# Kernel optimization log

Measured on AMD Instinct MI355X. Metric: run time of the kernel, lower is better.

## Reference

```python
import jax, jax.numpy as jnp
import numpy as np

B, T, D = 2, 2048, 2048
N, K, H = 16, 8, 128            # heads, kv heads, head_dim
SOFT_CAP = 50.0
WINDOW = 1024
SCALE = H ** -0.5               # query_pre_attn_scalar
ROPE_BASE = 10000.0
ROPE_SCALE = 1.0
K_MASK = -2.3819763e+38


def rms_norm(x, scale, eps=1e-6):
    var = jnp.mean(jnp.square(x), axis=-1, keepdims=True)
    return x * jax.lax.rsqrt(var + eps) * (1.0 + scale)


def apply_rope(x, positions):
    # x: [B,T,heads,H]; positions: [B,T] int
    head_dim = x.shape[-1]
    fraction = 2.0 * jnp.arange(head_dim // 2, dtype=jnp.float32) / head_dim
    timescale = ROPE_BASE ** fraction                      # [H/2]
    sinusoid = positions[..., None].astype(jnp.float32) / timescale  # [B,T,H/2]
    sinusoid = sinusoid[..., None, :] / ROPE_SCALE          # [B,T,1,H/2]
    sin, cos = jnp.sin(sinusoid), jnp.cos(sinusoid)
    first, second = jnp.split(x, 2, axis=-1)
    return jnp.concatenate([first * cos - second * sin,
                            second * cos + first * sin], axis=-1)


def setup_inputs() -> dict:
    key = jax.random.key(0)
    ks = jax.random.split(key, 6)
    x = jax.random.normal(ks[0], (B, T, D), jnp.float32)
    q_w = jax.random.normal(ks[1], (N, D, H), jnp.float32) * (D ** -0.5)
    kv_w = jax.random.normal(ks[2], (2, K, D, H), jnp.float32) * (D ** -0.5)
    o_w = jax.random.normal(ks[3], (N, H, D), jnp.float32) * ((N * H) ** -0.5)
    qnorm_scale = 0.1 * jax.random.normal(ks[4], (H,), jnp.float32)
    knorm_scale = 0.1 * jax.random.normal(ks[5], (H,), jnp.float32)
    segment_pos = jnp.broadcast_to(jnp.arange(T, dtype=jnp.int32), (B, T))
    attn_mask = jnp.broadcast_to(jnp.tril(jnp.ones((T, T), dtype=bool)), (B, T, T))
    return {"x": x, "q_w": q_w, "kv_w": kv_w, "o_w": o_w,
            "qnorm_scale": qnorm_scale, "knorm_scale": knorm_scale,
            "segment_pos": segment_pos, "attn_mask": attn_mask}


def reference(x, q_w, kv_w, o_w, qnorm_scale, knorm_scale, segment_pos, attn_mask):
    # projections
    q = jnp.einsum('BTD,NDH->BTNH', x, q_w)            # [B,T,N,H]
    k = jnp.einsum('BSD,KDH->BSKH', x, kv_w[0])        # [B,T,K,H]
    v = jnp.einsum('BSD,KDH->BSKH', x, kv_w[1])
    # QK RMSNorm, then RoPE, then query scaling (matches source order)
    q = apply_rope(rms_norm(q, qnorm_scale), segment_pos) * SCALE
    k = apply_rope(rms_norm(k, knorm_scale), segment_pos)
    # GQA: regroup query heads per kv head
    G = N // K
    qg = q.reshape(B, T, K, G, H)
    logits = jnp.einsum('BTKGH,BSKH->BTKGS', qg, k).reshape(B, T, N, T)
    # logit soft cap
    logits = jnp.tanh(logits / SOFT_CAP) * SOFT_CAP
    # sliding window mask combined with causal attn_mask
    pos_q = segment_pos[:, :, None]
    pos_k = segment_pos[:, None, :]
    sliding = (pos_k > pos_q - WINDOW) & (pos_k < pos_q + WINDOW)
    mask = attn_mask & sliding                          # [B,T,S]
    padded = jnp.where(mask[:, :, None, :], logits, K_MASK)
    probs = jax.nn.softmax(padded, axis=-1).astype(k.dtype)
    enc = jnp.einsum('BTKGS,BSKH->BTKGH',
                     probs.reshape(B, T, K, G, T), v).reshape(B, T, N, H)
    return jnp.einsum('BTNH,NHD->BTD', enc, o_w)
```

## Files before the change

### kernel.cpp

```cpp
#include <hip/hip_runtime.h>
#include <stdint.h>

#define BB 2
#define TT 2048
#define DD 2048
#define NHD 16
#define KVH 8
#define HD 128
#define JC 4096
#define WIN 1024
#define SCALE_Q 0.08838834764831845f

typedef __attribute__((ext_vector_type(8))) short bf16x8;
typedef __attribute__((ext_vector_type(8))) unsigned short us8;
typedef __attribute__((ext_vector_type(4))) unsigned short us4;
typedef __attribute__((ext_vector_type(4))) float f32x4;
typedef __attribute__((ext_vector_type(16))) float f32x16;
typedef __attribute__((ext_vector_type(4))) unsigned int u32x4;

#define GAS __attribute__((address_space(1)))
#define LAS __attribute__((address_space(3)))

__device__ __forceinline__ unsigned short f2bf(float f) {
  unsigned u = __float_as_uint(f);
  u += 0x7FFFu + ((u >> 16) & 1u);
  return (unsigned short)(u >> 16);
}
__device__ __forceinline__ float bf2f(unsigned short u) {
  return __uint_as_float(((unsigned)u) << 16);
}

__device__ __forceinline__ void gload16(const void* g, void* l) {
  __builtin_amdgcn_global_load_lds((const GAS unsigned int*)g, (LAS unsigned int*)l, 16, 0, 0);
}

#define VMCNT(n) asm volatile("s_waitcnt vmcnt(" #n ")" ::: "memory")

__global__ void __launch_bounds__(256) k_pre(
    const float4* __restrict__ x4, us4* __restrict__ xb,
    const float* __restrict__ qw, const float* __restrict__ kvw,
    const float* __restrict__ ow, unsigned short* __restrict__ Wt,
    unsigned short* __restrict__ Wt_o) {
  __shared__ float tile[32][33];
  int id = blockIdx.x;
  int tid = threadIdx.x;
  if (id < 8192) {
    int i = id * 256 + tid;
    float4 v = x4[i];
    us4 o;
    o[0] = f2bf(v.x); o[1] = f2bf(v.y); o[2] = f2bf(v.z); o[3] = f2bf(v.w);
    xb[i] = o;
    return;
  }
  const float* ib;
  unsigned short* ob;
  int ldin, c0, r0;
  int t = id - 8192;
  if (t < 8192) {
    int bx = t & 3, by = (t >> 2) & 63, z = t >> 8;
    ib = (z < 16) ? qw + (long)z * 2048 * 128 : kvw + (long)(z - 16) * 2048 * 128;
    ob = Wt + (long)z * 128 * 2048;
    ldin = 128;
    c0 = bx * 32; r0 = by * 32;
  } else {
    int u = t - 8192;
    ib = ow; ob = Wt_o; ldin = 2048;
    c0 = (u & 63) * 32; r0 = (u >> 6) * 32;
  }
  int tx = tid & 31, ty = tid >> 5;
#pragma unroll
  for (int i = 0; i < 4; i++)
    tile[ty + i * 8][tx] = ib[(long)(r0 + ty + i * 8) * ldin + c0 + tx];
  __syncthreads();
#pragma unroll
  for (int i = 0; i < 4; i++)
    ob[(long)(c0 + ty + i * 8) * 2048 + r0 + tx] = f2bf(tile[tx][ty + i * 8]);
}

template <int BM, int BN, int NWN, int THREADS, int NBUF, bool BF16OUT>
__global__ void __launch_bounds__(THREADS, 2) k_gemm9(
    const unsigned short* __restrict__ A, const unsigned short* __restrict__ Bt,
    void* __restrict__ Cv, int M, int Nn, int nby) {
  constexpr int KD = 2048;
  constexpr int NT = KD / 32;
  constexpr int ROWS = BM + BN;
  constexpr int RPI = THREADS / 4;
  constexpr int IA = BM / RPI;
  constexpr int IPT = ROWS / RPI;
  constexpr int MT = BM / 32;
  constexpr int MT2 = MT / 2;
  __shared__ short lds[NBUF][ROWS * 32];

  int tid = threadIdx.x, lane = tid & 63, w = tid >> 6;
  int wm = w / NWN, wn = w % NWN;
  int id = blockIdx.x;
  int cpx = gridDim.x >> 3;
  id = (id & 7) * cpx + (id >> 3);
  int m0 = (id / nby) * BM, n0 = (id % nby) * BN;

  int srow = tid >> 2;
  int scol = ((tid & 3) ^ ((tid >> 3) & 3)) * 8;
  const unsigned short* gA = A + (long)(m0 + srow) * KD + scol;
  const unsigned short* gB = Bt + (long)(n0 + srow) * KD + scol;

  auto STG = [&](int p, int ko, int j) {
    if (j < IA)
      gload16(gA + (long)j * RPI * KD + ko, &lds[p][(j * RPI + w * 16) * 32]);
    else
      gload16(gB + (long)(j - IA) * RPI * KD + ko,
              &lds[p][(BM + (j - IA) * RPI + w * 16) * 32]);
  };

  int frag = (lane & 15) * 32 + (((lane >> 4) ^ ((lane >> 1) & 3)) * 8);
  int abase = wm * (BM / 2) * 32 + frag;
  int bbase = (BM + wn * 64) * 32 + frag;

  f32x4 acc[MT][4] = {};
#pragma unroll
  for (int tt = 0; tt < NBUF - 1; ++tt)
#pragma unroll
    for (int j = 0; j < IPT; ++j) STG(tt, tt * 32, j);
  {
    constexpr int PW = IPT * (NBUF - 2);
    if constexpr (PW >= 8)      VMCNT(8);
    else if constexpr (PW == 6) VMCNT(6);
    else if constexpr (PW == 4) VMCNT(4);
    else                        VMCNT(0);
  }
  __builtin_amdgcn_s_barrier();

  int buf = 0, sp = NBUF - 1;
  for (int t = 0; t < NT; ++t) {
    const short* bufp = lds[buf];
    bool st = (t + NBUF - 1) < NT;
    int ko = (t + NBUF - 1) * 32;
    bf16x8 bfr[4], af[MT2];
#pragma unroll
    for (int ni = 0; ni < 4; ++ni)
      bfr[ni] = *(const bf16x8*)&bufp[bbase + ni * 16 * 32];
#pragma unroll
    for (int mi = 0; mi < MT2; ++mi)
      af[mi] = *(const bf16x8*)&bufp[abase + mi * 16 * 32];
    if (st) {
#pragma unroll
      for (int j = 0; j < IPT / 2; ++j) STG(sp, ko, j);
    }
    __builtin_amdgcn_s_barrier();
    asm volatile("s_waitcnt lgkmcnt(0)" ::: "memory");
    __builtin_amdgcn_sched_barrier(0);
    __builtin_amdgcn_s_setprio(1);
#pragma unroll
    for (int mi = 0; mi < MT2; ++mi)
#pragma unroll
      for (int ni = 0; ni < 4; ++ni)
        acc[mi][ni] = __builtin_amdgcn_mfma_f32_16x16x32_bf16(af[mi], bfr[ni], acc[mi][ni], 0, 0, 0);
    __builtin_amdgcn_s_setprio(0);
    __builtin_amdgcn_s_barrier();
    bf16x8 af2[MT2];
#pragma unroll
    for (int mi = 0; mi < MT2; ++mi)
      af2[mi] = *(const bf16x8*)&bufp[abase + (MT2 + mi) * 16 * 32];
    if (st) {
#pragma unroll
      for (int j = IPT / 2; j < IPT; ++j) STG(sp, ko, j);
    }
    {
      int rem = NT - 2 - t;
      if (rem > NBUF - 2) rem = NBUF - 2;
      if (rem == 2) {
        if constexpr (IPT == 4) VMCNT(8); else VMCNT(12);
      } else if (rem == 1) {
        if constexpr (IPT == 4) VMCNT(4); else VMCNT(6);
      } else if (rem == 0) {
        VMCNT(0);
      }
    }
    __builtin_amdgcn_s_barrier();
    asm volatile("s_waitcnt lgkmcnt(0)" ::: "memory");
    __builtin_amdgcn_sched_barrier(0);
    __builtin_amdgcn_s_setprio(1);
#pragma unroll
    for (int mi = 0; mi < MT2; ++mi)
#pragma unroll
      for (int ni = 0; ni < 4; ++ni)
        acc[MT2 + mi][ni] = __builtin_amdgcn_mfma_f32_16x16x32_bf16(af2[mi], bfr[ni], acc[MT2 + mi][ni], 0, 0, 0);
    __builtin_amdgcn_s_setprio(0);
    __builtin_amdgcn_s_barrier();
    buf = (buf == NBUF - 1) ? 0 : buf + 1;
    sp = (sp == NBUF - 1) ? 0 : sp + 1;
  }

#pragma unroll
  for (int mi = 0; mi < MT; mi++)
#pragma unroll
    for (int ni = 0; ni < 4; ni++)
#pragma unroll
      for (int r = 0; r < 4; r++) {
        int row = m0 + wm * (BM / 2) + mi * 16 + (lane >> 4) * 4 + r;
        int col = n0 + wn * 64 + ni * 16 + (lane & 15);
        if constexpr (BF16OUT)
          ((unsigned short*)Cv)[(long)row * Nn + col] = f2bf(acc[mi][ni][r]);
        else
          ((float*)Cv)[(long)row * Nn + col] = acc[mi][ni][r];
      }
}

__global__ void __launch_bounds__(256) k_post(
    const unsigned short* __restrict__ qkv, const float* __restrict__ qns,
    const float* __restrict__ kns, unsigned short* __restrict__ qb,
    unsigned short* __restrict__ kb, unsigned short* __restrict__ vbT) {
  int id = blockIdx.x;
  int tid = threadIdx.x;
  if (id < 24576) {
    int wid = tid >> 6, lane = tid & 63;
    long r = (long)id * 4 + wid;
    int b = (int)(r / (TT * 24));
    int rem = (int)(r % (TT * 24));
    int t = rem / 24, hd = rem % 24;
    const unsigned short* row = qkv + (long)(b * TT + t) * JC + (hd < 16 ? hd * HD : 2048 + (hd - 16) * HD);
    float f0 = bf2f(row[lane]), f1 = bf2f(row[lane + 64]);
    float ss = f0 * f0 + f1 * f1;
#pragma unroll
    for (int m = 1; m < 64; m <<= 1) ss += __shfl_xor(ss, m, 64);
    float rinv = rsqrtf(ss * (1.0f / 128.0f) + 1e-6f);
    const float* sc = (hd < 16) ? qns : kns;
    float y0 = f0 * rinv * (1.0f + sc[lane]);
    float y1 = f1 * rinv * (1.0f + sc[lane + 64]);
    float ts = exp2f((float)lane * (13.287712379549449f / 64.0f));
    float ang = (float)t / ts;
    float s, c;
    sincosf(ang, &s, &c);
    float o0 = y0 * c - y1 * s;
    float o1 = y1 * c + y0 * s;
    unsigned short* dst;
    if (hd < 16) {
      o0 *= SCALE_Q; o1 *= SCALE_Q;
      dst = qb + ((long)(b * NHD + hd) * TT + t) * HD;
    } else {
      dst = kb + ((long)(b * KVH + (hd - 16)) * TT + t) * HD;
    }
    dst[lane] = f2bf(o0);
    dst[lane + 64] = f2bf(o1);
    return;
  }
  __shared__ unsigned short tile[32][33];
  int t4 = id - 24576;
  int bx = t4 & 3, by = (t4 >> 2) & 63, z = t4 >> 8;
  const unsigned short* ib = qkv + 3072 + (long)(z / 8) * 2048 * 4096 + (long)(z % 8) * 128;
  unsigned short* ob = vbT + (long)z * 128 * 2048;
  int c0 = bx * 32, r0 = by * 32;
  int tx = tid & 31, ty = tid >> 5;
#pragma unroll
  for (int i = 0; i < 4; i++)
    tile[ty + i * 8][tx] = ib[(long)(r0 + ty + i * 8) * 4096 + c0 + tx];
  __syncthreads();
#pragma unroll
  for (int i = 0; i < 4; i++)
    ob[(long)(c0 + ty + i * 8) * 2048 + r0 + tx] = tile[tx][ty + i * 8];
}

template <bool FULL>
__device__ __forceinline__ void softcap16(const f32x16& s16, float* pr, float& lsum,
                                          int s_base, int tq, int g) {
#pragma unroll
  for (int r = 0; r < 16; r++) {
    float x = s16[r];
    float e2 = __builtin_amdgcn_exp2f(0.05770780163555853f * x);
    float p = __builtin_amdgcn_exp2f(-144.26950408889634f * __builtin_amdgcn_rcpf(1.0f + e2));
    if (!FULL) {
      int s = s_base + (r & 3) + 8 * (r >> 2) + 4 * g;
      bool valid = (s <= tq) && (s > tq - WIN);
      p = valid ? p : 0.0f;
    }
    lsum += p;
    pr[r] = p;
  }
}

__device__ __forceinline__ void hswap(unsigned& a, unsigned& b, int g) {
  unsigned ax = (unsigned)__shfl_xor((int)a, 32, 64);
  unsigned bx = (unsigned)__shfl_xor((int)b, 32, 64);
  unsigned r0 = g ? bx : a;
  unsigned r1 = g ? b : ax;
  a = r0; b = r1;
}

__global__ void __launch_bounds__(256, 2) k_attn(
    const unsigned short* __restrict__ qb, const unsigned short* __restrict__ kb,
    const unsigned short* __restrict__ vbT, unsigned short* __restrict__ enc) {
  __shared__ short Kl[2][64][128];
  __shared__ short Vt[2][128][64];
  int tid = threadIdx.x, lane = tid & 63, w = tid >> 6;
  int g = lane >> 5, l31 = lane & 31;
  int id = blockIdx.x;
  int b = id >> 8;
  int rem = id & 255;
  int n = rem >> 4;
  int traw = rem & 15;
  int tile = b ? ((traw + 8) & 15) : traw;
  int t0 = tile * 128;
  int kh = n >> 1;
  const unsigned short* qbase = qb + ((long)(b * NHD + n) * TT + t0 + w * 32) * HD;
  const unsigned short* kbase = kb + (long)(b * KVH + kh) * TT * HD;
  const unsigned short* vbase = vbT + (long)(b * KVH + kh) * HD * TT;

  bf16x8 bq[8];
  {
    const unsigned short* qp = qbase + (long)l31 * HD + g * 8;
#pragma unroll
    for (int kb8 = 0; kb8 < 8; kb8++)
      bq[kb8] = *(const bf16x8*)(qp + kb8 * 16);
  }

  f32x16 acc[4] = {};
  float lsum = 0.0f;
  int t0w = t0 + w * 32;
  int tq = t0w + l31;
  int s_begin = (t0 >= WIN) ? t0 - WIN : 0;
  int s_end = t0 + 128;

  auto STAGE = [&](int buf, int s0) {
#pragma unroll
    for (int i = 0; i < 4; i++) {
      int row = w * 16 + i * 4 + (lane >> 4);
      int c16 = (lane & 15) ^ (row & 7);
      gload16(kbase + (long)(s0 + row) * HD + c16 * 8, &Kl[buf][w * 16 + i * 4][0]);
    }
#pragma unroll
    for (int i = 0; i < 4; i++) {
      int row = w * 32 + i * 8 + (lane >> 3);
      int c16 = (lane & 7) ^ (row & 7);
      gload16(vbase + (long)row * TT + s0 + c16 * 8, &Vt[buf][w * 32 + i * 8][0]);
    }
  };

  STAGE(0, s_begin);
  __syncthreads();
  int cur = 0;
  for (int s0 = s_begin; s0 < s_end; s0 += 64) {
    if (s0 + 64 < s_end) STAGE(cur ^ 1, s0 + 64);
    bool live = (s0 <= t0w + 31) && (s0 + 63 >= t0w - (WIN - 1));
    if (live) {
      f32x16 sc2[2] = {};
#pragma unroll
      for (int sb = 0; sb < 2; sb++) {
        int srow = sb * 32 + l31;
#pragma unroll
        for (int kb8 = 0; kb8 < 8; kb8++) {
          bf16x8 ak = *(const bf16x8*)&Kl[cur][srow][8 * ((2 * kb8 + g) ^ (srow & 7))];
          sc2[sb] = __builtin_amdgcn_mfma_f32_32x32x16_bf16(ak, bq[kb8], sc2[sb], 0, 0, 0);
        }
      }
      bool full = (s0 + 63 <= t0w) && (s0 >= t0w + 31 - (WIN - 1));
      unsigned pw[4][4];
#pragma unroll
      for (int sb = 0; sb < 2; sb++) {
        float pr[16];
        if (full) softcap16<true>(sc2[sb], pr, lsum, 0, tq, g);
        else      softcap16<false>(sc2[sb], pr, lsum, s0 + sb * 32, tq, g);
        unsigned X[4], Y[4];
#pragma unroll
        for (int m = 0; m < 4; m++) {
          asm("v_cvt_pk_bf16_f32 %0, %1, %2" : "=v"(X[m]) : "v"(pr[4 * m]), "v"(pr[4 * m + 1]));
          asm("v_cvt_pk_bf16_f32 %0, %1, %2" : "=v"(Y[m]) : "v"(pr[4 * m + 2]), "v"(pr[4 * m + 3]));
        }
#pragma unroll
        for (int kl = 0; kl < 2; kl++) {
          hswap(X[2 * kl], X[2 * kl + 1], g);
          hswap(Y[2 * kl], Y[2 * kl + 1], g);
          pw[sb * 2 + kl][0] = X[2 * kl];
          pw[sb * 2 + kl][1] = Y[2 * kl];
          pw[sb * 2 + kl][2] = X[2 * kl + 1];
          pw[sb * 2 + kl][3] = Y[2 * kl + 1];
        }
      }
#pragma unroll
      for (int ks = 0; ks < 4; ks++) {
        u32x4 t4 = {pw[ks][0], pw[ks][1], pw[ks][2], pw[ks][3]};
        bf16x8 pb = __builtin_bit_cast(bf16x8, t4);
#pragma unroll
        for (int ht = 0; ht < 4; ht++) {
          int hrow = ht * 32 + l31;
          bf16x8 av = *(const bf16x8*)&Vt[cur][hrow][8 * ((2 * ks + g) ^ (hrow & 7))];
          acc[ht] = __builtin_amdgcn_mfma_f32_32x32x16_bf16(av, pb, acc[ht], 0, 0, 0);
        }
      }
    }
    __syncthreads();
    cur ^= 1;
  }

  lsum += __shfl_xor(lsum, 32, 64);
  float inv = __builtin_amdgcn_rcpf(lsum);
  unsigned short* dst = enc + ((long)(b * TT + tq) * NHD + n) * HD;
#pragma unroll
  for (int ht = 0; ht < 4; ht++)
#pragma unroll
    for (int r4 = 0; r4 < 4; r4++) {
      us4 o;
#pragma unroll
      for (int e = 0; e < 4; e++) o[e] = f2bf(acc[ht][r4 * 4 + e] * inv);
      *(us4*)(dst + ht * 32 + 8 * r4 + 4 * g) = o;
    }
}

extern "C" void kernel_launch(void* const* d_in, const int* in_sizes, int n_in,
                              void* d_out, int out_size, void* d_ws, size_t ws_size,
                              hipStream_t stream) {
  const float* x    = (const float*)d_in[0];
  const float* q_w  = (const float*)d_in[1];
  const float* kv_w = (const float*)d_in[2];
  const float* o_w  = (const float*)d_in[3];
  const float* qns  = (const float*)d_in[4];
  const float* kns  = (const float*)d_in[5];

  if (ws_size < (104ull << 20)) return;
  char* ws = (char*)d_ws;
  unsigned short* qkvb = (unsigned short*)(ws + 0);
  unsigned short* enc  = (unsigned short*)(ws + 0);
  unsigned short* x_bf = (unsigned short*)(ws + (64ll << 20));
  unsigned short* qb   = (unsigned short*)(ws + (64ll << 20));
  unsigned short* Wt   = (unsigned short*)(ws + (80ll << 20));
  unsigned short* kb   = (unsigned short*)(ws + (80ll << 20));
  unsigned short* vbT  = (unsigned short*)(ws + (88ll << 20));
  unsigned short* Wt_o = (unsigned short*)(ws + (96ll << 20));

  k_pre<<<20480, 256, 0, stream>>>((const float4*)x, (us4*)x_bf, q_w, kv_w, o_w, Wt, Wt_o);
  k_gemm9<256, 128, 2, 256, 3, true><<<512, 256, 0, stream>>>(x_bf, Wt, qkvb, 4096, 4096, 32);
  k_post<<<28672, 256, 0, stream>>>(qkvb, qns, kns, qb, kb, vbT);
  k_attn<<<512, 256, 0, stream>>>(qb, kb, vbT, enc);
  k_gemm9<128, 128, 2, 256, 3, false><<<512, 256, 0, stream>>>(enc, Wt_o, (float*)d_out, 4096, 2048, 16);
}
```

Before: 218.6 us.

## Replace QKV projection GEMM with 256x256-tile, 8-wave ping-pong pipelined kernel

Adds a new bf16 GEMM kernel for the fused QKV projection. It uses 256x256 output tiles, 512 threads (8 waves), a K-step of 64 and two LDS stages. Global loads for future K-steps are staggered across four sub-phases of each iteration, interleaved with MFMA blocks under s_setprio and barriers. It also adds an XCD-aware block remap and XOR-swizzled LDS to avoid bank conflicts. The goal is more data reuse per tile and better overlap of memory and compute, at the cost of heavy register pressure from 128 accumulators per lane and fewer blocks in the grid.

After: 210.6 us. 1.04x faster.

```diff
diff --git a/kernel.cpp b/kernel.cpp
--- a/kernel.cpp
+++ b/kernel.cpp
@@ -75,6 +75,108 @@
 #pragma unroll
   for (int i = 0; i < 4; i++)
     ob[(long)(c0 + ty + i * 8) * 2048 + r0 + tx] = f2bf(tile[tx][ty + i * 8]);
+}
+
+template <bool BF16OUT>
+__global__ void __launch_bounds__(512, 2) k_gemm8p(
+    const unsigned short* __restrict__ A, const unsigned short* __restrict__ Bt,
+    void* __restrict__ Cv, int Nn, int nby) {
+  constexpr int KD = 2048;
+  constexpr int NT = KD / 64;
+  __shared__ short lds[2 * 4 * 8192];
+
+  int tid = threadIdx.x, lane = tid & 63, w = tid >> 6;
+  int wm = w >> 2, wn = w & 3;
+  int id = blockIdx.x;
+  int cpx = gridDim.x >> 3;
+  id = (id & 7) * cpx + (id >> 3);
+  int m0 = (id / nby) * 256, n0 = (id % nby) * 256;
+
+  int srow = tid >> 3;
+  int scol = ((tid & 7) ^ ((tid >> 3) & 7)) * 8;
+  const unsigned short* gA = A + (long)(m0 + srow) * KD + scol;
+  const unsigned short* gB = Bt + (long)(n0 + srow) * KD + scol;
+  int wrow = w * 8 * 64;
+
+  auto STG = [&](int p, int ko, int r) {
+    const unsigned short* gsrc = (r < 2) ? gA + (long)(r * 128) * KD + ko
+                                         : gB + (long)((r - 2) * 128) * KD + ko;
+    short* dst = &lds[p * 32768 + r * 8192 + wrow];
+#pragma unroll
+    for (int i = 0; i < 2; ++i)
+      gload16(gsrc + (long)(i * 64) * KD, dst + i * 4096);
+  };
+
+  int c0 = ((lane >> 4) ^ (lane & 7)) * 8;
+  int abase = wm * 8192 + (lane & 15) * 64;
+  int bbase = 16384 + (wn >> 1) * 8192 + ((wn & 1) * 64 + (lane & 15)) * 64;
+
+  f32x4 acc[8][4] = {};
+#pragma unroll
+  for (int r = 0; r < 4; ++r) STG(0, 0, r);
+  STG(1, 64, 2);
+  STG(1, 64, 3);
+  VMCNT(4);
+  __builtin_amdgcn_s_barrier();
+
+  bf16x8 bf[4][2];
+  for (int t = 0; t < NT; ++t) {
+    const short* bp = &lds[(t & 1) * 32768];
+    int sb1 = (t + 1) & 1, sb2 = t & 1;
+    int ko1 = (t + 1) * 64, ko2 = (t + 2) * 64;
+    bool s1 = (t + 1) < NT, s2 = (t + 2) < NT;
+#pragma unroll
+    for (int q = 0; q < 4; ++q) {
+      bf16x8 af[2][2];
+#pragma unroll
+      for (int m2 = 0; m2 < 2; ++m2)
+#pragma unroll
+        for (int kk = 0; kk < 2; ++kk)
+          af[m2][kk] = *(const bf16x8*)&bp[abase + (q * 2 + m2) * 16 * 64 + (c0 ^ (kk * 32))];
+      if (q == 0) {
+#pragma unroll
+        for (int ni = 0; ni < 4; ++ni)
+#pragma unroll
+          for (int kk = 0; kk < 2; ++kk)
+            bf[ni][kk] = *(const bf16x8*)&bp[bbase + ni * 16 * 64 + (c0 ^ (kk * 32))];
+      }
+      if (q == 0) { if (s1) STG(sb1, ko1, 0); }
+      else if (q == 1) { if (s1) STG(sb1, ko1, 1); }
+      else if (q == 2) { if (s2) STG(sb2, ko2, 2); }
+      else {
+        if (s2) { STG(sb2, ko2, 3); VMCNT(4); }
+        else if (s1) VMCNT(0);
+      }
+      __builtin_amdgcn_s_barrier();
+      asm volatile("s_waitcnt lgkmcnt(0)" ::: "memory");
+      __builtin_amdgcn_sched_barrier(0);
+      __builtin_amdgcn_s_setprio(1);
+#pragma unroll
+      for (int m2 = 0; m2 < 2; ++m2)
+#pragma unroll
+        for (int ni = 0; ni < 4; ++ni)
+#pragma unroll
+          for (int kk = 0; kk < 2; ++kk)
+            acc[q * 2 + m2][ni] = __builtin_amdgcn_mfma_f32_16x16x32_bf16(
+                af[m2][kk], bf[ni][kk], acc[q * 2 + m2][ni], 0, 0, 0);
+      __builtin_amdgcn_s_setprio(0);
+      __builtin_amdgcn_s_barrier();
+    }
+  }
+
+#pragma unroll
+  for (int mi = 0; mi < 8; mi++)
+#pragma unroll
+    for (int ni = 0; ni < 4; ni++)
+#pragma unroll
+      for (int r = 0; r < 4; r++) {
+        int row = m0 + wm * 128 + mi * 16 + (lane >> 4) * 4 + r;
+        int col = n0 + wn * 64 + ni * 16 + (lane & 15);
+        if constexpr (BF16OUT)
+          ((unsigned short*)Cv)[(long)row * Nn + col] = f2bf(acc[mi][ni][r]);
+        else
+          ((float*)Cv)[(long)row * Nn + col] = acc[mi][ni][r];
+      }
 }
 
 template <int BM, int BN, int NWN, int THREADS, int NBUF, bool BF16OUT>
@@ -426,7 +528,7 @@
   unsigned short* Wt_o = (unsigned short*)(ws + (96ll << 20));
 
   k_pre<<<20480, 256, 0, stream>>>((const float4*)x, (us4*)x_bf, q_w, kv_w, o_w, Wt, Wt_o);
-  k_gemm9<256, 128, 2, 256, 3, true><<<512, 256, 0, stream>>>(x_bf, Wt, qkvb, 4096, 4096, 32);
+  k_gemm8p<true><<<256, 512, 0, stream>>>(x_bf, Wt, qkvb, 4096, 16);
   k_post<<<28672, 256, 0, stream>>>(qkvb, qns, kns, qb, kb, vbT);
   k_attn<<<512, 256, 0, stream>>>(qb, kb, vbT, enc);
   k_gemm9<128, 128, 2, 256, 3, false><<<512, 256, 0, stream>>>(enc, Wt_o, (float*)d_out, 4096, 2048, 16);
```
